# Optimization experiments

Measured on AMD Instinct MI355X. Metric: run time of the kernel, lower is better.

## Reference

```python
import jax, jax.numpy as jnp
import numpy as np

B, L, S, D = 64, 1024, 8, 128  # batch, seq len, num_snapshots, feat dim


def setup_inputs() -> dict:
    key = jax.random.key(0)
    ks = jax.random.split(key, 12)
    src_ids = jax.random.randint(ks[0], (B, L), 0, 2000, dtype=jnp.int32)
    dst_ids = jax.random.randint(ks[1], (B, L), 0, 2000, dtype=jnp.int32)
    # snapshot ids are 1..S in the original code (indexing uses snaps - 1)
    src_snaps = jax.random.randint(ks[2], (B, L), 1, S + 1, dtype=jnp.int32)
    dst_snaps = jax.random.randint(ks[3], (B, L), 1, S + 1, dtype=jnp.int32)
    def lin(k, fan_in, shape):
        return jax.random.uniform(k, shape, jnp.float32, -1.0, 1.0) / np.sqrt(fan_in)
    params = {
        # AggregateSnapshots MLP: Linear(S, D) -> ReLU -> Linear(D, 2)
        'agg_w1': lin(ks[4], S, (S, D)), 'agg_b1': lin(ks[5], S, (D,)),
        'agg_w2': lin(ks[6], D, (D, 2)), 'agg_b2': lin(ks[7], D, (2,)),
        # neighbor_intersect_encode_layer: Linear(1, D) -> ReLU -> Linear(D, D)
        'enc_w1': lin(ks[8], 1, (1, D)), 'enc_b1': lin(ks[9], 1, (D,)),
        'enc_w2': lin(ks[10], D, (D, D)), 'enc_b2': lin(ks[11], D, (D,)),
    }
    return dict(src_padded_nodes_neighbor_ids=src_ids,
                dst_padded_nodes_neighbor_ids=dst_ids,
                src_padded_nodes_snapshots=src_snaps,
                dst_padded_nodes_snapshots=dst_snaps,
                num_snapshots=S, **params)


def _match_counts(ids_a, sn_a, ids_b, sn_b):
    # counts[i, j] = #{k : ids_b[i,k] == ids_a[i,j] and sn_b[i,k] == sn_a[i,j]}
    eq = (ids_a[:, :, None] == ids_b[:, None, :]) & (sn_a[:, :, None] == sn_b[:, None, :])
    return eq.sum(axis=-1).astype(jnp.float32)  # [B, L]


def _intersects(ids, sn, other_ids, other_sn, num_snapshots):
    self_cnt = _match_counts(ids, sn, ids, sn)            # [B, L]
    cross_cnt = _match_counts(ids, sn, other_ids, other_sn)
    valid = (ids != 0).astype(jnp.float32)                # padding rows stay zero
    oh = jax.nn.one_hot(sn - 1, num_snapshots, dtype=jnp.float32)  # [B, L, S]
    cnts = jnp.stack([self_cnt, cross_cnt], axis=2)       # [B, L, 2]
    return (cnts * valid[:, :, None])[..., None] * oh[:, :, None, :]  # [B, L, 2, S]


def _agg_mlp(x, w1, b1, w2, b2):
    # x: [B, L, 2, S] -> Linear(S,D) -> ReLU -> Linear(D,2) -> reshape(B,L,2,2) -> mean over dim 2
    h = jax.nn.relu(jnp.einsum('blcs,sd->blcd', x, w1) + b1)
    y = jnp.einsum('blcd,de->blce', h, w2) + b2           # [B, L, 2, 2]
    return y.mean(axis=2)                                 # [B, L, 2]


def _encode(y, w1, b1, w2, b2):
    # y: [B, L, 2] -> unsqueeze(-1) -> Linear(1,D) -> ReLU -> Linear(D,D) -> sum over dim 2
    h = jax.nn.relu(y[..., None] * w1[0] + b1)            # [B, L, 2, D]
    z = jnp.einsum('blcd,de->blce', h, w2) + b2
    return z.sum(axis=2)                                  # [B, L, D]


def reference(src_padded_nodes_neighbor_ids, dst_padded_nodes_neighbor_ids,
              src_padded_nodes_snapshots, dst_padded_nodes_snapshots, num_snapshots,
              agg_w1, agg_b1, agg_w2, agg_b2, enc_w1, enc_b1, enc_w2, enc_b2):
    src_int = _intersects(src_padded_nodes_neighbor_ids, src_padded_nodes_snapshots,
                          dst_padded_nodes_neighbor_ids, dst_padded_nodes_snapshots, num_snapshots)
    dst_self_cross = _intersects(dst_padded_nodes_neighbor_ids, dst_padded_nodes_snapshots,
                                 src_padded_nodes_neighbor_ids, src_padded_nodes_snapshots, num_snapshots)
    # dst layout: channel 0 = counts from src list, channel 1 = self counts
    dst_int = dst_self_cross[:, :, ::-1, :]
    src_snap_feat = _agg_mlp(src_int, agg_w1, agg_b1, agg_w2, agg_b2)
    dst_snap_feat = _agg_mlp(dst_int, agg_w1, agg_b1, agg_w2, agg_b2)
    src_feat = _encode(src_snap_feat, enc_w1, enc_b1, enc_w2, enc_b2)
    dst_feat = _encode(dst_snap_feat, enc_w1, enc_b1, enc_w2, enc_b2)
    return (src_feat, dst_feat)
```

## Files before the change

### kernel.cpp

```cpp
#include <hip/hip_runtime.h>


#define LSEQ    1024
#define NBATCH  64
#define DDIM    128
#define NKEYS   16384
#define CMAX    16
#define NUNITS  (2 * NBATCH * LSEQ)
#define NQUADS  (NUNITS * (DDIM / 4))

__global__ __launch_bounds__(1024) void prep_kernel(
    const int* __restrict__ src_ids, const int* __restrict__ dst_ids,
    const int* __restrict__ src_sn,  const int* __restrict__ dst_sn,
    const float* __restrict__ agg_w1, const float* __restrict__ agg_b1,
    const float* __restrict__ agg_w2, const float* __restrict__ agg_b2,
    const float* __restrict__ enc_w1, const float* __restrict__ enc_b1,
    const float* __restrict__ enc_w2, const float* __restrict__ enc_b2,
    unsigned int* __restrict__ rowinfo, float* __restrict__ table)
{
    __shared__ unsigned int hist[NKEYS];

    if (blockIdx.x < NBATCH) {
        const int b = blockIdx.x;
        const int t = threadIdx.x;

        uint4* h4 = (uint4*)hist;
        const uint4 z = make_uint4(0u, 0u, 0u, 0u);
        #pragma unroll
        for (int i = 0; i < NKEYS / 4 / 1024; ++i) h4[t + i * 1024] = z;
        __syncthreads();

        const int base = b * LSEQ;
        const int sid = src_ids[base + t];
        const int ssn = src_sn[base + t];
        const int did = dst_ids[base + t];
        const int dsn = dst_sn[base + t];

        const unsigned int ssnz = (unsigned int)((ssn - 1) & 7);
        const unsigned int dsnz = (unsigned int)((dsn - 1) & 7);
        unsigned int skey = (unsigned int)(sid * 8) + ssnz;
        unsigned int dkey = (unsigned int)(did * 8) + dsnz;
        if (skey >= NKEYS) skey = NKEYS - 1;
        if (dkey >= NKEYS) dkey = NKEYS - 1;

        atomicAdd(&hist[skey], 1u);
        atomicAdd(&hist[dkey], 65536u);
        __syncthreads();

        const unsigned int hs = hist[skey];
        const unsigned int hd = hist[dkey];
        const unsigned int sv = (sid != 0) ? 1u : 0u;
        const unsigned int dv = (did != 0) ? 1u : 0u;
        const unsigned int sc0 = (hs & 0xffffu) * sv;
        const unsigned int sc1 = (hs >> 16) * sv;
        const unsigned int dc0 = (hd >> 16) * dv;
        const unsigned int dc1 = (hd & 0xffffu) * dv;

        unsigned int si, di;
        if (sc0 < CMAX && sc1 < CMAX)
            si = (ssnz << 8) | (sc0 << 4) | sc1;
        else
            si = 0x80000000u | sc0 | (sc1 << 11) | (ssnz << 22);
        if (dc0 < CMAX && dc1 < CMAX)
            di = (dsnz << 8) | (dc0 << 4) | dc1;
        else
            di = 0x80000000u | dc0 | (dc1 << 11) | (dsnz << 22);

        rowinfo[base + t]                   = si;
        rowinfo[NBATCH * LSEQ + base + t]   = di;
    } else {
        const int wave = threadIdx.x >> 6;
        const int lane = threadIdx.x & 63;
        const int r = (blockIdx.x - NBATCH) * 16 + wave;
        const int sn = r >> 8;
        const int c0 = (r >> 4) & 15;
        const int c1 = r & 15;

        float p0 = 0.0f, p1 = 0.0f;
        #pragma unroll
        for (int half = 0; half < 2; ++half) {
            const int d = lane + half * 64;
            const float w1d = agg_w1[sn * DDIM + d];
            const float b1d = agg_b1[d];
            const float h = fmaxf((float)c0 * w1d + b1d, 0.0f)
                          + fmaxf((float)c1 * w1d + b1d, 0.0f);
            p0 += h * agg_w2[d * 2 + 0];
            p1 += h * agg_w2[d * 2 + 1];
        }
        #pragma unroll
        for (int m = 32; m; m >>= 1) {
            p0 += __shfl_xor(p0, m, 64);
            p1 += __shfl_xor(p1, m, 64);
        }
        const float y0 = agg_b2[0] + 0.5f * p0;
        const float y1 = agg_b2[1] + 0.5f * p1;

        float a0 = 2.0f * enc_b2[lane];
        float a1 = 2.0f * enc_b2[lane + 64];
        #pragma unroll 4
        for (int k = 0; k < DDIM; ++k) {
            const float w1e = enc_w1[k], b1e = enc_b1[k];
            const float gk = fmaxf(y0 * w1e + b1e, 0.0f)
                           + fmaxf(y1 * w1e + b1e, 0.0f);
            a0 += gk * enc_w2[k * DDIM + lane];
            a1 += gk * enc_w2[k * DDIM + lane + 64];
        }
        table[r * DDIM + lane]      = a0;
        table[r * DDIM + lane + 64] = a1;
    }
}

__device__ __noinline__ void slow_path(
    unsigned int info, int q,
    const float* __restrict__ agg_w1, const float* __restrict__ agg_b1,
    const float* __restrict__ agg_w2, const float* __restrict__ agg_b2,
    const float* __restrict__ enc_w1, const float* __restrict__ enc_b1,
    const float* __restrict__ enc_w2, const float* __restrict__ enc_b2,
    float4* v)
{
    const unsigned int c0  = info & 0x7FFu;
    const unsigned int c1  = (info >> 11) & 0x7FFu;
    const unsigned int snz = (info >> 22) & 7u;
    float s0 = 0.0f, s1 = 0.0f;
    for (int dd = 0; dd < DDIM; ++dd) {
        const float w1d = agg_w1[snz * DDIM + dd];
        const float b1d = agg_b1[dd];
        const float h = fmaxf((float)c0 * w1d + b1d, 0.0f)
                      + fmaxf((float)c1 * w1d + b1d, 0.0f);
        s0 += h * agg_w2[dd * 2 + 0];
        s1 += h * agg_w2[dd * 2 + 1];
    }
    const float y0 = agg_b2[0] + 0.5f * s0;
    const float y1 = agg_b2[1] + 0.5f * s1;
    float o0 = 2.0f * enc_b2[q * 4 + 0];
    float o1 = 2.0f * enc_b2[q * 4 + 1];
    float o2 = 2.0f * enc_b2[q * 4 + 2];
    float o3 = 2.0f * enc_b2[q * 4 + 3];
    for (int k = 0; k < DDIM; ++k) {
        const float w1e = enc_w1[k], b1e = enc_b1[k];
        const float gk = fmaxf(y0 * w1e + b1e, 0.0f)
                       + fmaxf(y1 * w1e + b1e, 0.0f);
        o0 += gk * enc_w2[k * DDIM + q * 4 + 0];
        o1 += gk * enc_w2[k * DDIM + q * 4 + 1];
        o2 += gk * enc_w2[k * DDIM + q * 4 + 2];
        o3 += gk * enc_w2[k * DDIM + q * 4 + 3];
    }
    *v = make_float4(o0, o1, o2, o3);
}

__global__ __launch_bounds__(256) void gather_kernel(
    const unsigned int* __restrict__ rowinfo,
    const float* __restrict__ table,
    const float* __restrict__ agg_w1, const float* __restrict__ agg_b1,
    const float* __restrict__ agg_w2, const float* __restrict__ agg_b2,
    const float* __restrict__ enc_w1, const float* __restrict__ enc_b1,
    const float* __restrict__ enc_w2, const float* __restrict__ enc_b2,
    float* __restrict__ out)
{
    const float4* table4 = (const float4*)table;
    float4* out4 = (float4*)out;
    const int base = blockIdx.x * 1024 + threadIdx.x;

    #pragma unroll
    for (int k = 0; k < 4; ++k) {
        const int gt   = base + k * 256;
        const int unit = gt >> 5;
        const int q    = gt & 31;
        const unsigned int info = rowinfo[unit];
        float4 v;
        if (!(info & 0x80000000u)) {
            v = table4[(info << 5) + q];
        } else {
            slow_path(info, q, agg_w1, agg_b1, agg_w2, agg_b2,
                      enc_w1, enc_b1, enc_w2, enc_b2, &v);
        }
        __builtin_nontemporal_store(v.x, &out4[gt].x);
        __builtin_nontemporal_store(v.y, &out4[gt].y);
        __builtin_nontemporal_store(v.z, &out4[gt].z);
        __builtin_nontemporal_store(v.w, &out4[gt].w);
    }
}

extern "C" void kernel_launch(void* const* d_in, const int* in_sizes, int n_in,
                              void* d_out, int out_size, void* d_ws, size_t ws_size,
                              hipStream_t stream)
{
    const int* src_ids = (const int*)d_in[0];
    const int* dst_ids = (const int*)d_in[1];
    const int* src_sn  = (const int*)d_in[2];
    const int* dst_sn  = (const int*)d_in[3];
    const float* agg_w1 = (const float*)d_in[5];
    const float* agg_b1 = (const float*)d_in[6];
    const float* agg_w2 = (const float*)d_in[7];
    const float* agg_b2 = (const float*)d_in[8];
    const float* enc_w1 = (const float*)d_in[9];
    const float* enc_b1 = (const float*)d_in[10];
    const float* enc_w2 = (const float*)d_in[11];
    const float* enc_b2 = (const float*)d_in[12];
    float* out = (float*)d_out;

    unsigned int* rowinfo = (unsigned int*)d_ws;
    float* table = (float*)(rowinfo + NUNITS);

    prep_kernel<<<NBATCH + 128, 1024, 0, stream>>>(
        src_ids, dst_ids, src_sn, dst_sn,
        agg_w1, agg_b1, agg_w2, agg_b2,
        enc_w1, enc_b1, enc_w2, enc_b2,
        rowinfo, table);

    gather_kernel<<<NQUADS / 1024, 256, 0, stream>>>(
        rowinfo, table,
        agg_w1, agg_b1, agg_w2, agg_b2,
        enc_w1, enc_b1, enc_w2, enc_b2, out);
}
```

Measured before the change: 126.5 us.

## Move rare large-count rows to a separate fixup kernel, branchless gather

Rows whose match counts exceed the precomputed table range are now clamped into the table index and also recorded in a per-batch slow list during prep. The gather kernel becomes a branch-free table copy with vector nontemporal stores. A third kernel recomputes the listed rows and overwrites their output. This removes the noinline slow-path call and divergence from the hot gather loop, at the cost of an extra kernel launch and some redundant writes for overflow rows.

```diff
diff --git a/kernel.cpp b/kernel.cpp
--- a/kernel.cpp
+++ b/kernel.cpp
@@ -9,6 +9,12 @@
 #define NUNITS  (2 * NBATCH * LSEQ)
 #define NQUADS  (NUNITS * (DDIM / 4))
 
+typedef float f4 __attribute__((ext_vector_type(4)));
+
+__device__ __forceinline__ unsigned int umin_u(unsigned int a, unsigned int b) {
+    return a < b ? a : b;
+}
+
 __global__ __launch_bounds__(1024) void prep_kernel(
     const int* __restrict__ src_ids, const int* __restrict__ dst_ids,
     const int* __restrict__ src_sn,  const int* __restrict__ dst_sn,
@@ -16,9 +22,11 @@
     const float* __restrict__ agg_w2, const float* __restrict__ agg_b2,
     const float* __restrict__ enc_w1, const float* __restrict__ enc_b1,
     const float* __restrict__ enc_w2, const float* __restrict__ enc_b2,
-    unsigned int* __restrict__ rowinfo, float* __restrict__ table)
+    unsigned int* __restrict__ rowinfo, float* __restrict__ table,
+    unsigned int* __restrict__ slowcnt, uint2* __restrict__ slowbuf)
 {
     __shared__ unsigned int hist[NKEYS];
+    __shared__ unsigned int slot;
 
     if (blockIdx.x < NBATCH) {
         const int b = blockIdx.x;
@@ -28,6 +36,7 @@
         const uint4 z = make_uint4(0u, 0u, 0u, 0u);
         #pragma unroll
         for (int i = 0; i < NKEYS / 4 / 1024; ++i) h4[t + i * 1024] = z;
+        if (t == 0) slot = 0u;
         __syncthreads();
 
         const int base = b * LSEQ;
@@ -56,18 +65,25 @@
         const unsigned int dc0 = (hd >> 16) * dv;
         const unsigned int dc1 = (hd & 0xffffu) * dv;
 
-        unsigned int si, di;
-        if (sc0 < CMAX && sc1 < CMAX)
-            si = (ssnz << 8) | (sc0 << 4) | sc1;
-        else
-            si = 0x80000000u | sc0 | (sc1 << 11) | (ssnz << 22);
-        if (dc0 < CMAX && dc1 < CMAX)
-            di = (dsnz << 8) | (dc0 << 4) | dc1;
-        else
-            di = 0x80000000u | dc0 | (dc1 << 11) | (dsnz << 22);
-
-        rowinfo[base + t]                   = si;
-        rowinfo[NBATCH * LSEQ + base + t]   = di;
+        rowinfo[base + t] =
+            (ssnz << 8) | (umin_u(sc0, CMAX - 1) << 4) | umin_u(sc1, CMAX - 1);
+        rowinfo[NBATCH * LSEQ + base + t] =
+            (dsnz << 8) | (umin_u(dc0, CMAX - 1) << 4) | umin_u(dc1, CMAX - 1);
+
+        if (sc0 >= CMAX || sc1 >= CMAX) {
+            const unsigned int e = atomicAdd(&slot, 1u);
+            slowbuf[b * 2048 + e] =
+                make_uint2((unsigned int)(base + t),
+                           sc0 | (sc1 << 11) | (ssnz << 22));
+        }
+        if (dc0 >= CMAX || dc1 >= CMAX) {
+            const unsigned int e = atomicAdd(&slot, 1u);
+            slowbuf[b * 2048 + e] =
+                make_uint2((unsigned int)(NBATCH * LSEQ + base + t),
+                           dc0 | (dc1 << 11) | (dsnz << 22));
+        }
+        __syncthreads();
+        if (t == 0) slowcnt[b] = slot;
     } else {
         const int wave = threadIdx.x >> 6;
         const int lane = threadIdx.x & 63;
@@ -110,74 +126,73 @@
     }
 }
 
-__device__ __noinline__ void slow_path(
-    unsigned int info, int q,
-    const float* __restrict__ agg_w1, const float* __restrict__ agg_b1,
-    const float* __restrict__ agg_w2, const float* __restrict__ agg_b2,
-    const float* __restrict__ enc_w1, const float* __restrict__ enc_b1,
-    const float* __restrict__ enc_w2, const float* __restrict__ enc_b2,
-    float4* v)
-{
-    const unsigned int c0  = info & 0x7FFu;
-    const unsigned int c1  = (info >> 11) & 0x7FFu;
-    const unsigned int snz = (info >> 22) & 7u;
-    float s0 = 0.0f, s1 = 0.0f;
-    for (int dd = 0; dd < DDIM; ++dd) {
-        const float w1d = agg_w1[snz * DDIM + dd];
-        const float b1d = agg_b1[dd];
-        const float h = fmaxf((float)c0 * w1d + b1d, 0.0f)
-                      + fmaxf((float)c1 * w1d + b1d, 0.0f);
-        s0 += h * agg_w2[dd * 2 + 0];
-        s1 += h * agg_w2[dd * 2 + 1];
-    }
-    const float y0 = agg_b2[0] + 0.5f * s0;
-    const float y1 = agg_b2[1] + 0.5f * s1;
-    float o0 = 2.0f * enc_b2[q * 4 + 0];
-    float o1 = 2.0f * enc_b2[q * 4 + 1];
-    float o2 = 2.0f * enc_b2[q * 4 + 2];
-    float o3 = 2.0f * enc_b2[q * 4 + 3];
-    for (int k = 0; k < DDIM; ++k) {
-        const float w1e = enc_w1[k], b1e = enc_b1[k];
-        const float gk = fmaxf(y0 * w1e + b1e, 0.0f)
-                       + fmaxf(y1 * w1e + b1e, 0.0f);
-        o0 += gk * enc_w2[k * DDIM + q * 4 + 0];
-        o1 += gk * enc_w2[k * DDIM + q * 4 + 1];
-        o2 += gk * enc_w2[k * DDIM + q * 4 + 2];
-        o3 += gk * enc_w2[k * DDIM + q * 4 + 3];
-    }
-    *v = make_float4(o0, o1, o2, o3);
-}
-
 __global__ __launch_bounds__(256) void gather_kernel(
     const unsigned int* __restrict__ rowinfo,
     const float* __restrict__ table,
+    float* __restrict__ out)
+{
+    const f4* table4 = (const f4*)table;
+    f4* out4 = (f4*)out;
+    const int base = blockIdx.x * 1024 + threadIdx.x;
+
+    #pragma unroll
+    for (int k = 0; k < 4; ++k) {
+        const int gt = base + k * 256;
+        const unsigned int info = rowinfo[gt >> 5];
+        const f4 v = table4[(info << 5) + (gt & 31)];
+        __builtin_nontemporal_store(v, &out4[gt]);
+    }
+}
+
+__global__ __launch_bounds__(256) void fixup_kernel(
+    const unsigned int* __restrict__ slowcnt,
+    const uint2* __restrict__ slowbuf,
     const float* __restrict__ agg_w1, const float* __restrict__ agg_b1,
     const float* __restrict__ agg_w2, const float* __restrict__ agg_b2,
     const float* __restrict__ enc_w1, const float* __restrict__ enc_b1,
     const float* __restrict__ enc_w2, const float* __restrict__ enc_b2,
     float* __restrict__ out)
 {
-    const float4* table4 = (const float4*)table;
-    float4* out4 = (float4*)out;
-    const int base = blockIdx.x * 1024 + threadIdx.x;
-
-    #pragma unroll
-    for (int k = 0; k < 4; ++k) {
-        const int gt   = base + k * 256;
-        const int unit = gt >> 5;
-        const int q    = gt & 31;
-        const unsigned int info = rowinfo[unit];
-        float4 v;
-        if (!(info & 0x80000000u)) {
-            v = table4[(info << 5) + q];
-        } else {
-            slow_path(info, q, agg_w1, agg_b1, agg_w2, agg_b2,
-                      enc_w1, enc_b1, enc_w2, enc_b2, &v);
-        }
-        __builtin_nontemporal_store(v.x, &out4[gt].x);
-        __builtin_nontemporal_store(v.y, &out4[gt].y);
-        __builtin_nontemporal_store(v.z, &out4[gt].z);
-        __builtin_nontemporal_store(v.w, &out4[gt].w);
+    const int b = blockIdx.x;
+    const unsigned int n = slowcnt[b];
+    if (n == 0u) return;
+
+    const int q = threadIdx.x & 31;
+    f4* out4 = (f4*)out;
+    for (unsigned int e0 = 0; e0 < n; e0 += 8) {
+        const unsigned int e = e0 + (threadIdx.x >> 5);
+        if (e >= n) continue;
+        const uint2 ent = slowbuf[b * 2048 + e];
+        const unsigned int c0  = ent.y & 0x7FFu;
+        const unsigned int c1  = (ent.y >> 11) & 0x7FFu;
+        const unsigned int snz = (ent.y >> 22) & 7u;
+
+        float s0 = 0.0f, s1 = 0.0f;
+        for (int dd = 0; dd < DDIM; ++dd) {
+            const float w1d = agg_w1[snz * DDIM + dd];
+            const float b1d = agg_b1[dd];
+            const float h = fmaxf((float)c0 * w1d + b1d, 0.0f)
+                          + fmaxf((float)c1 * w1d + b1d, 0.0f);
+            s0 += h * agg_w2[dd * 2 + 0];
+            s1 += h * agg_w2[dd * 2 + 1];
+        }
+        const float y0 = agg_b2[0] + 0.5f * s0;
+        const float y1 = agg_b2[1] + 0.5f * s1;
+        f4 v;
+        v.x = 2.0f * enc_b2[q * 4 + 0];
+        v.y = 2.0f * enc_b2[q * 4 + 1];
+        v.z = 2.0f * enc_b2[q * 4 + 2];
+        v.w = 2.0f * enc_b2[q * 4 + 3];
+        for (int k = 0; k < DDIM; ++k) {
+            const float w1e = enc_w1[k], b1e = enc_b1[k];
+            const float gk = fmaxf(y0 * w1e + b1e, 0.0f)
+                           + fmaxf(y1 * w1e + b1e, 0.0f);
+            v.x += gk * enc_w2[k * DDIM + q * 4 + 0];
+            v.y += gk * enc_w2[k * DDIM + q * 4 + 1];
+            v.z += gk * enc_w2[k * DDIM + q * 4 + 2];
+            v.w += gk * enc_w2[k * DDIM + q * 4 + 3];
+        }
+        out4[ent.x * 32u + q] = v;
     }
 }
 
@@ -201,15 +216,19 @@
 
     unsigned int* rowinfo = (unsigned int*)d_ws;
     float* table = (float*)(rowinfo + NUNITS);
+    unsigned int* slowcnt = (unsigned int*)(table + 2048 * DDIM);
+    uint2* slowbuf = (uint2*)(slowcnt + 64);
 
     prep_kernel<<<NBATCH + 128, 1024, 0, stream>>>(
         src_ids, dst_ids, src_sn, dst_sn,
         agg_w1, agg_b1, agg_w2, agg_b2,
         enc_w1, enc_b1, enc_w2, enc_b2,
-        rowinfo, table);
-
-    gather_kernel<<<NQUADS / 1024, 256, 0, stream>>>(
-        rowinfo, table,
+        rowinfo, table, slowcnt, slowbuf);
+
+    gather_kernel<<<NQUADS / 1024, 256, 0, stream>>>(rowinfo, table, out);
+
+    fixup_kernel<<<NBATCH, 256, 0, stream>>>(
+        slowcnt, slowbuf,
         agg_w1, agg_b1, agg_w2, agg_b2,
         enc_w1, enc_b1, enc_w2, enc_b2, out);
 }
```

Measured after the change: 114.6 us. 1.1x faster.
